# Optimization experiments

Measured on AMD Instinct MI355X. Metric: run time of the kernel, lower is better.

Reference implementation:

```python
import jax, jax.numpy as jnp
import numpy as np
import math

K = 2
CAPACITY = -1
NEED_L_AUX = True


def topk_gating(logits, k=K, capacity=CAPACITY, need_l_aux=NEED_L_AUX):
    # logits: (T, P, E) tokens x prototypes x experts-per-prototype
    gates = jax.nn.softmax(logits.astype(jnp.float32), axis=-1).astype(logits.dtype)
    T, P, E = gates.shape
    cap = int(math.ceil(1.25 * T / E)) if capacity < 0 else capacity

    idx1 = jnp.argmax(gates, axis=-1)                      # (T, P)
    mask1 = jax.nn.one_hot(idx1, E, dtype=jnp.int32)       # (T, P, E)
    loc1 = jnp.cumsum(mask1, axis=0) - 1                   # position in expert queue
    if need_l_aux:
        me = jnp.mean(gates, axis=0)
        ce = jnp.mean(mask1.astype(jnp.float32), axis=0)
        l_aux = jnp.mean(me * ce)
    else:
        l_aux = jnp.zeros((), jnp.float32)
    mask1 = mask1 * (loc1 < cap)                           # drop over-capacity tokens
    loc1_s = jnp.sum(loc1 * mask1, axis=-1)                # (T, P)
    gates1_s = jnp.sum(gates * mask1, axis=-1)
    denom = gates1_s
    gates_s_list = [gates1_s]
    mask_list = [mask1]
    loc_s_list = [loc1_s]
    last_logits = logits
    last_mask = mask1
    prev_masks = mask1
    for _ in range(2, k + 1):
        last_logits = jnp.where(last_mask.astype(bool), -jnp.inf, last_logits)
        idx = jnp.argmax(last_logits, axis=-1)
        mask = jax.nn.one_hot(idx, E, dtype=jnp.int32)
        loc = jnp.cumsum(mask, axis=0) - 1 + jnp.sum(prev_masks, axis=0, keepdims=True)
        mask = mask * (loc < cap)
        last_mask = mask
        prev_masks = prev_masks + mask
        mask_list.append(mask)
        loc_s_list.append(jnp.sum(loc * mask, axis=-1))
        gs = jnp.sum(gates * mask, axis=-1)
        denom = denom + gs
        gates_s_list.append(gs)
    denom = jnp.maximum(denom, jnp.finfo(denom.dtype).eps)

    combine = jnp.zeros((T, P, E, cap), gates.dtype)
    for gs, mask, ls in zip(gates_s_list, mask_list, loc_s_list):
        g = (gs / denom)[..., None] * mask                  # (T, P, E)
        loc_sc = jax.nn.one_hot(ls, cap, dtype=gates.dtype)  # (T, P, cap)
        combine = combine + g[..., None] * loc_sc[:, :, None, :]
    dispatch_mask = combine.astype(bool)
    return l_aux.astype(logits.dtype), combine.astype(logits.dtype), dispatch_mask


def setup_inputs() -> dict:
    key = jax.random.key(0)
    k1, k2 = jax.random.split(key)
    inp = jax.random.normal(k1, (4096, 2048), dtype=jnp.float32)
    W = jax.random.normal(k2, (64, 2048), dtype=jnp.float32) / math.sqrt(2048.0)
    return {"input": inp, "W": W, "bs": 4096, "prototypes": 2}


def reference(input, W, bs, prototypes):
    logits = input @ W.T                                   # (T, num_experts_total)
    logits = logits.reshape(input.shape[0], prototypes, -1)  # (T, P, E)
    return topk_gating(logits, k=K, capacity=CAPACITY, need_l_aux=NEED_L_AUX)
```

## Files before the change

### kernel.cpp

```cpp
#include <hip/hip_runtime.h>
#include <cstdint>

#define T_TOK 4096
#define KDIM 2048
#define NE 64
#define NP 2
#define EE 32
#define CAP 160
#define NKC 8
#define KCHUNK 256
#define BLKR 128
#define COMB_ELEMS 41943040ull
#define OUT_ELEMS 83886081ull
#define SMALLF 65536

__global__ __launch_bounds__(256) void k_gemm(const float* __restrict__ x,
                                              const float* __restrict__ W,
                                              float* __restrict__ part) {
  __shared__ float xs[BLKR][36];
  __shared__ float wt[32][68];
  const int tid = threadIdx.x;
  const int rb = blockIdx.x & 31;
  const int kc = blockIdx.x >> 5;
  const int r0 = rb * BLKR;
  const int er = tid & 15;
  const int rg = tid >> 4;
  float acc[8][4];
#pragma unroll
  for (int i = 0; i < 8; ++i)
#pragma unroll
    for (int c = 0; c < 4; ++c) acc[i][c] = 0.f;

  float4 sx[4], sw[2];
  {
    const int kb = kc * KCHUNK;
#pragma unroll
    for (int q = 0; q < 4; ++q) {
      const int li = tid + q * 256, row = li >> 3, kq = (li & 7) * 4;
      sx[q] = *reinterpret_cast<const float4*>(&x[(size_t)(r0 + row) * KDIM + kb + kq]);
    }
#pragma unroll
    for (int q = 0; q < 2; ++q) {
      const int li = tid + q * 256, e = li >> 3, kq = (li & 7) * 4;
      sw[q] = *reinterpret_cast<const float4*>(&W[(size_t)e * KDIM + kb + kq]);
    }
  }
  for (int s = 0; s < 8; ++s) {
    __syncthreads();
#pragma unroll
    for (int q = 0; q < 4; ++q) {
      const int li = tid + q * 256, row = li >> 3, kq = (li & 7) * 4;
      *reinterpret_cast<float4*>(&xs[row][kq]) = sx[q];
    }
#pragma unroll
    for (int q = 0; q < 2; ++q) {
      const int li = tid + q * 256, e = li >> 3, kq = (li & 7) * 4;
      wt[kq][e] = sw[q].x; wt[kq + 1][e] = sw[q].y;
      wt[kq + 2][e] = sw[q].z; wt[kq + 3][e] = sw[q].w;
    }
    if (s < 7) {
      const int kb = kc * KCHUNK + (s + 1) * 32;
#pragma unroll
      for (int q = 0; q < 4; ++q) {
        const int li = tid + q * 256, row = li >> 3, kq = (li & 7) * 4;
        sx[q] = *reinterpret_cast<const float4*>(&x[(size_t)(r0 + row) * KDIM + kb + kq]);
      }
#pragma unroll
      for (int q = 0; q < 2; ++q) {
        const int li = tid + q * 256, e = li >> 3, kq = (li & 7) * 4;
        sw[q] = *reinterpret_cast<const float4*>(&W[(size_t)e * KDIM + kb + kq]);
      }
    }
    __syncthreads();
#pragma unroll
    for (int k4 = 0; k4 < 8; ++k4) {
      float4 wb[4];
#pragma unroll
      for (int j = 0; j < 4; ++j)
        wb[j] = *reinterpret_cast<const float4*>(&wt[k4 * 4 + j][er * 4]);
#pragma unroll
      for (int i = 0; i < 8; ++i) {
        const float4 xv = *reinterpret_cast<const float4*>(&xs[rg + 16 * i][k4 * 4]);
        acc[i][0] = fmaf(xv.w, wb[3].x, fmaf(xv.z, wb[2].x, fmaf(xv.y, wb[1].x, fmaf(xv.x, wb[0].x, acc[i][0]))));
        acc[i][1] = fmaf(xv.w, wb[3].y, fmaf(xv.z, wb[2].y, fmaf(xv.y, wb[1].y, fmaf(xv.x, wb[0].y, acc[i][1]))));
        acc[i][2] = fmaf(xv.w, wb[3].z, fmaf(xv.z, wb[2].z, fmaf(xv.y, wb[1].z, fmaf(xv.x, wb[0].z, acc[i][2]))));
        acc[i][3] = fmaf(xv.w, wb[3].w, fmaf(xv.z, wb[2].w, fmaf(xv.y, wb[1].w, fmaf(xv.x, wb[0].w, acc[i][3]))));
      }
    }
  }
#pragma unroll
  for (int i = 0; i < 8; ++i) {
    float4 v; v.x = acc[i][0]; v.y = acc[i][1]; v.z = acc[i][2]; v.w = acc[i][3];
    *reinterpret_cast<float4*>(
        &part[((size_t)kc * T_TOK + r0 + rg + 16 * i) * NE + er * 4]) = v;
  }
}

__global__ __launch_bounds__(64) void k_soft(const float* __restrict__ part,
                                             float2* __restrict__ g12,
                                             int* __restrict__ idxs,
                                             float* __restrict__ me_part) {
  __shared__ float lg[64][33];
  const int tid = threadIdx.x;
  const int R = blockIdx.x * 64 + tid;
  const int t = R >> 1;
  const int p = R & 1;
  float v[32];
  const float* pr = part + (size_t)t * NE + p * EE;
#pragma unroll
  for (int e = 0; e < 32; e += 4) {
    float4 s = *reinterpret_cast<const float4*>(pr + e);
    v[e] = s.x; v[e + 1] = s.y; v[e + 2] = s.z; v[e + 3] = s.w;
  }
  for (int kc = 1; kc < NKC; ++kc) {
    const float* prk = pr + (size_t)kc * T_TOK * NE;
#pragma unroll
    for (int e = 0; e < 32; e += 4) {
      float4 s = *reinterpret_cast<const float4*>(prk + e);
      v[e] += s.x; v[e + 1] += s.y; v[e + 2] += s.z; v[e + 3] += s.w;
    }
  }
  float m = v[0];
#pragma unroll
  for (int e = 1; e < 32; ++e) m = fmaxf(m, v[e]);
  float sum = 0.f;
#pragma unroll
  for (int e = 0; e < 32; ++e) { v[e] = expf(v[e] - m); sum += v[e]; }
  const float inv = 1.0f / sum;
#pragma unroll
  for (int e = 0; e < 32; ++e) v[e] *= inv;
  float g1 = -1.f; int i1 = 0;
#pragma unroll
  for (int e = 0; e < 32; ++e) if (v[e] > g1) { g1 = v[e]; i1 = e; }
  float g2 = -1.f; int i2 = 0;
#pragma unroll
  for (int e = 0; e < 32; ++e) if (e != i1 && v[e] > g2) { g2 = v[e]; i2 = e; }
  g12[R] = make_float2(g1, g2);
  idxs[R] = i1 | (i2 << 8);
#pragma unroll
  for (int e = 0; e < 32; ++e) lg[tid][e] = v[e];
  __syncthreads();
  {
    const int pp = tid >> 5, ee = tid & 31;
    float s = 0.f;
    for (int rr = pp; rr < 64; rr += 2) s += lg[rr][ee];
    me_part[blockIdx.x * 64 + tid] = s;
  }
}

__global__ __launch_bounds__(1024) void k_scan(const int* __restrict__ idxs,
                                               const float2* __restrict__ g12,
                                               const float* __restrict__ me_part,
                                               int2* __restrict__ fl,
                                               float2* __restrict__ wvp,
                                               float* __restrict__ out) {
  __shared__ int grp[NP][64][32];
  __shared__ int tot[NP][32];
  __shared__ unsigned short tk1[NP][T_TOK];
  __shared__ unsigned short tk2[NP][T_TOK];
  __shared__ float red[64];
  const int tid = threadIdx.x;
  const int wvi = tid >> 6;
  const int p = wvi >> 3;
  const int wg = wvi & 7;
  const int l = tid & 63;
  const unsigned long long lmask = (1ull << l) - 1ull;
  for (int gi = 0; gi < 8; ++gi) {
    const int g = wg * 8 + gi;
    const int t = g * 64 + l;
    const int e1 = idxs[t * 2 + p] & 255;
    if (l < 32) grp[p][g][l] = 0;
    unsigned long long m = ~0ull;
#pragma unroll
    for (int b = 0; b < 5; ++b) {
      const unsigned long long bm = __ballot((e1 >> b) & 1);
      m &= ((e1 >> b) & 1) ? bm : ~bm;
    }
    const int rank = (int)__popcll(m & lmask);
    if (rank == 0) grp[p][g][e1] = (int)__popcll(m);
    tk1[p][t] = (unsigned short)(rank | (e1 << 6));
  }
  __syncthreads();
  if (tid < 64) {
    const int pp = tid >> 5, ee = tid & 31;
    int s = 0;
    for (int g = 0; g < 64; ++g) { int vv = grp[pp][g][ee]; grp[pp][g][ee] = s; s += vv; }
    tot[pp][ee] = s;
  }
  __syncthreads();
  for (int gi = 0; gi < 8; ++gi) {
    const int g = wg * 8 + gi;
    const int t = g * 64 + l;
    const int vv = tk1[p][t];
    tk1[p][t] = (unsigned short)(grp[p][g][vv >> 6] + (vv & 63));
  }
  if (tid < 64) {
    float s = 0.f;
    for (int b = 0; b < 128; ++b) s += me_part[b * 64 + tid];
    red[tid] = s * (float)tot[tid >> 5][tid & 31];
  }
  __syncthreads();
  if (tid == 0) {
    float s = 0.f;
    for (int i = 0; i < 64; ++i) s += red[i];
    out[0] = s / (64.0f * 4096.0f * 4096.0f);
  }
  for (int gi = 0; gi < 8; ++gi) {
    const int g = wg * 8 + gi;
    const int t = g * 64 + l;
    const int ii = idxs[t * 2 + p];
    const int e2 = (tk1[p][t] < CAP) ? (ii >> 8) : (ii & 255);
    if (l < 32) grp[p][g][l] = 0;
    unsigned long long m = ~0ull;
#pragma unroll
    for (int b = 0; b < 5; ++b) {
      const unsigned long long bm = __ballot((e2 >> b) & 1);
      m &= ((e2 >> b) & 1) ? bm : ~bm;
    }
    const int rank = (int)__popcll(m & lmask);
    if (rank == 0) grp[p][g][e2] = (int)__popcll(m);
    tk2[p][t] = (unsigned short)(rank | (e2 << 6));
  }
  __syncthreads();
  if (tid < 64) {
    const int pp = tid >> 5, ee = tid & 31;
    int s = min(tot[pp][ee], CAP);
    for (int g = 0; g < 64; ++g) { int vv = grp[pp][g][ee]; grp[pp][g][ee] = s; s += vv; }
  }
  __syncthreads();
  for (int gi = 0; gi < 8; ++gi) {
    const int g = wg * 8 + gi;
    const int t = g * 64 + l;
    const int R = t * 2 + p;
    const int ii = idxs[R];
    const int e1 = ii & 255;
    const int loc1v = tk1[p][t];
    const bool kept1 = loc1v < CAP;
    const int v2 = tk2[p][t];
    const int rank2 = v2 & 63, e2 = v2 >> 6;
    const int loc2 = grp[p][g][e2] + rank2;
    const bool kept2 = loc2 < CAP;
    const float2 gg = g12[R];
    const float gs1 = kept1 ? gg.x : 0.f;
    const float g2v = kept1 ? gg.y : gg.x;
    const float gs2 = kept2 ? g2v : 0.f;
    const float den = fmaxf(gs1 + gs2, 1.1920929e-07f);
    fl[R] = make_int2(kept1 ? e1 * CAP + loc1v : -1, kept2 ? e2 * CAP + loc2 : -1);
    wvp[R] = make_float2(gs1 / den, gs2 / den);
  }
}

__global__ __launch_bounds__(256) void k_write(const int2* __restrict__ fl,
                                               const float2* __restrict__ wvp,
                                               float* __restrict__ out,
                                               int nfullB) {
  const int b = blockIdx.x;
  const int tid = threadIdx.x;
  const int region = b >> 12;
  const int bd = b & 4095;
  if (region && bd >= nfullB) return;
  int fpos = -1; float fval = 0.f; size_t faddr = 0;
  if (tid < 4) {
    const int rr = 2 * bd + (tid >> 1);
    const int2 f = fl[rr];
    const float2 w = wvp[rr];
    const int which = tid & 1;
    fpos = which ? f.y : f.x;
    fval = region ? 1.0f : (which ? w.y : w.x);
    faddr = 1ull + (region ? COMB_ELEMS : 0ull) + (size_t)rr * 5120 + (size_t)(fpos < 0 ? 0 : fpos);
  }
  const size_t base = 1 + (region ? COMB_ELEMS : 0ull) + (size_t)bd * 10240;
  float4* p4 = (float4*)(out + base + 3);
  const float4 z4 = make_float4(0.f, 0.f, 0.f, 0.f);
#pragma unroll
  for (int j = 0; j < 10; ++j) {
    const int idx = tid + j * 256;
    if (idx < 2559) p4[idx] = z4;
  }
  if (tid < 3) out[base + tid] = 0.f;
  if (tid == 3) out[base + 10239] = 0.f;
  __syncthreads();
  if (tid < 4 && fpos >= 0) out[faddr] = fval;
}

__global__ __launch_bounds__(1024) void k_write_tail(const int2* __restrict__ fl,
                                                     float* __restrict__ out,
                                                     int nfullB) {
  __shared__ int2 sfl[16];
  const int tid = threadIdx.x;
  const int rstart = nfullB * 2;
  const int nr = 8192 - rstart;
  if (tid < nr) sfl[tid] = fl[rstart + tid];
  __syncthreads();
  const size_t base = 1 + COMB_ELEMS + (size_t)rstart * 5120;
  const int cnt = nr * 5120;
  const int nx4 = (cnt - 4) >> 2;
  float4* p4 = (float4*)(out + base + 3);
  const float4 z4 = make_float4(0.f, 0.f, 0.f, 0.f);
  for (int idx = tid; idx < nx4; idx += 1024) p4[idx] = z4;
  if (tid < 3) out[base + tid] = 0.f;
  if (tid == 3) out[base + cnt - 1] = 0.f;
  __syncthreads();
  if (tid < 2 * nr) {
    const int rr = rstart + (tid >> 1);
    const int2 f = sfl[tid >> 1];
    const int pos = (tid & 1) ? f.y : f.x;
    if (pos >= 0) out[1 + COMB_ELEMS + (size_t)rr * 5120 + pos] = 1.0f;
  }
}

extern "C" void kernel_launch(void* const* d_in, const int* in_sizes, int n_in,
                              void* d_out, int out_size, void* d_ws, size_t ws_size,
                              hipStream_t stream) {
  const float* x = (const float*)d_in[0];
  const float* W = (const float*)d_in[1];
  float* out = (float*)d_out;

  const size_t PARTF = (size_t)NKC * T_TOK * NE;

  float* small;
  float* part;
  int nfullB = 4096;
  if (ws_size >= (SMALLF + PARTF) * sizeof(float)) {
    small = (float*)d_ws;
    part = small + SMALLF;
  } else if (ws_size >= SMALLF * sizeof(float)) {
    small = (float*)d_ws;
    part = out + 4;
  } else {
    const size_t tb = (OUT_ELEMS - SMALLF) & ~(size_t)3;
    small = out + tb;
    part = out + 4;
    nfullB = (int)((tb - 1 - COMB_ELEMS) / 10240);
  }
  float2* g12 = (float2*)small;
  int* idxs = (int*)(small + 16384);
  float* me_part = small + 24576;
  int2* fl = (int2*)(small + 32768);
  float2* wvp = (float2*)(small + 49152);

  hipLaunchKernelGGL(k_gemm, dim3(256), dim3(256), 0, stream, x, W, part);
  hipLaunchKernelGGL(k_soft, dim3(128), dim3(64), 0, stream, part, g12, idxs, me_part);
  hipLaunchKernelGGL(k_scan, dim3(1), dim3(1024), 0, stream, idxs, g12, me_part, fl, wvp, out);
  hipLaunchKernelGGL(k_write, dim3(8192), dim3(256), 0, stream, fl, wvp, out, nfullB);
  if (nfullB < 4096)
    hipLaunchKernelGGL(k_write_tail, dim3(1), dim3(1024), 0, stream, fl, out, nfullB);
}
```

Measured before the change: 123.3 us.

## Overlap output zero-fill with GEMM blocks and scatter nonzeros in a separate fix kernel

Appends 4096 zero-fill blocks to the GEMM launch so the large combine/dispatch zeroing runs alongside the GEMM instead of after the scan. The old write kernel, which zeroed each row and then wrote the nonzeros, becomes a small scatter kernel that writes only the nonzero entries. Regions of the output that are reused as scratch are skipped and zeroed later by an extra fill kernel. The risks are that fill blocks compete with GEMM blocks for bandwidth and that the scratch aliasing paths are now more complex.

```diff
diff --git a/kernel.cpp b/kernel.cpp
--- a/kernel.cpp
+++ b/kernel.cpp
@@ -13,13 +13,33 @@
 #define COMB_ELEMS 41943040ull
 #define OUT_ELEMS 83886081ull
 #define SMALLF 65536
-
-__global__ __launch_bounds__(256) void k_gemm(const float* __restrict__ x,
-                                              const float* __restrict__ W,
-                                              float* __restrict__ part) {
+#define NFB 4096
+#define TOT4 20971520
+
+__global__ __launch_bounds__(256) void k_fused(const float* __restrict__ x,
+                                               const float* __restrict__ W,
+                                               float* __restrict__ part,
+                                               float* __restrict__ out,
+                                               int s1lo, int s1hi, int s2lo, int s2hi,
+                                               int fillLast) {
   __shared__ float xs[BLKR][36];
   __shared__ float wt[32][68];
   const int tid = threadIdx.x;
+  if (blockIdx.x >= 256) {
+    const int fb = blockIdx.x - 256;
+    float4* p4 = reinterpret_cast<float4*>(out);
+    const float4 z4 = make_float4(0.f, 0.f, 0.f, 0.f);
+    const int start = fb * 5120;
+#pragma unroll
+    for (int j = 0; j < 20; ++j) {
+      const int i4 = start + tid + j * 256;
+      if (i4 >= s1lo && i4 < s1hi) continue;
+      if (i4 >= s2lo && i4 < s2hi) continue;
+      p4[i4] = z4;
+    }
+    if (fillLast && fb == NFB - 1 && tid == 255) out[OUT_ELEMS - 1] = 0.f;
+    return;
+  }
   const int rb = blockIdx.x & 31;
   const int kc = blockIdx.x >> 5;
   const int r0 = rb * BLKR;
@@ -94,6 +114,14 @@
     *reinterpret_cast<float4*>(
         &part[((size_t)kc * T_TOK + r0 + rg + 16 * i) * NE + er * 4]) = v;
   }
+}
+
+__global__ __launch_bounds__(256) void k_fill2(float* __restrict__ out) {
+  float4* p4 = reinterpret_cast<float4*>(out + 4);
+  const float4 z4 = make_float4(0.f, 0.f, 0.f, 0.f);
+  const int base = blockIdx.x * 2048 + threadIdx.x;
+#pragma unroll
+  for (int j = 0; j < 8; ++j) p4[base + j * 256] = z4;
 }
 
 __global__ __launch_bounds__(64) void k_soft(const float* __restrict__ part,
@@ -250,37 +278,21 @@
   }
 }
 
-__global__ __launch_bounds__(256) void k_write(const int2* __restrict__ fl,
-                                               const float2* __restrict__ wvp,
-                                               float* __restrict__ out,
-                                               int nfullB) {
-  const int b = blockIdx.x;
-  const int tid = threadIdx.x;
-  const int region = b >> 12;
-  const int bd = b & 4095;
-  if (region && bd >= nfullB) return;
-  int fpos = -1; float fval = 0.f; size_t faddr = 0;
-  if (tid < 4) {
-    const int rr = 2 * bd + (tid >> 1);
-    const int2 f = fl[rr];
-    const float2 w = wvp[rr];
-    const int which = tid & 1;
-    fpos = which ? f.y : f.x;
-    fval = region ? 1.0f : (which ? w.y : w.x);
-    faddr = 1ull + (region ? COMB_ELEMS : 0ull) + (size_t)rr * 5120 + (size_t)(fpos < 0 ? 0 : fpos);
-  }
-  const size_t base = 1 + (region ? COMB_ELEMS : 0ull) + (size_t)bd * 10240;
-  float4* p4 = (float4*)(out + base + 3);
-  const float4 z4 = make_float4(0.f, 0.f, 0.f, 0.f);
-#pragma unroll
-  for (int j = 0; j < 10; ++j) {
-    const int idx = tid + j * 256;
-    if (idx < 2559) p4[idx] = z4;
-  }
-  if (tid < 3) out[base + tid] = 0.f;
-  if (tid == 3) out[base + 10239] = 0.f;
-  __syncthreads();
-  if (tid < 4 && fpos >= 0) out[faddr] = fval;
+__global__ __launch_bounds__(256) void k_fix(const int2* __restrict__ fl,
+                                             const float2* __restrict__ wvp,
+                                             float* __restrict__ out,
+                                             int rlimit) {
+  const int R = blockIdx.x * 256 + threadIdx.x;
+  const int2 f = fl[R];
+  const float2 w = wvp[R];
+  float* oc = out + 1 + (size_t)R * 5120;
+  if (f.x >= 0) oc[f.x] = w.x;
+  if (f.y >= 0) oc[f.y] = w.y;
+  if (R < rlimit) {
+    float* od = out + 1 + COMB_ELEMS + (size_t)R * 5120;
+    if (f.x >= 0) od[f.x] = 1.0f;
+    if (f.y >= 0) od[f.y] = 1.0f;
+  }
 }
 
 __global__ __launch_bounds__(1024) void k_write_tail(const int2* __restrict__ fl,
@@ -320,18 +332,27 @@
 
   float* small;
   float* part;
-  int nfullB = 4096;
+  int s1lo = 0, s1hi = 0, s2lo = 0, s2hi = 0, fillLast = 1;
+  bool needFill2 = false;
+  int nfullB = 4096, rlimit = 8192;
   if (ws_size >= (SMALLF + PARTF) * sizeof(float)) {
     small = (float*)d_ws;
     part = small + SMALLF;
   } else if (ws_size >= SMALLF * sizeof(float)) {
     small = (float*)d_ws;
     part = out + 4;
+    s1lo = 1; s1hi = 1 + (int)(PARTF / 4);
+    needFill2 = true;
   } else {
     const size_t tb = (OUT_ELEMS - SMALLF) & ~(size_t)3;
     small = out + tb;
     part = out + 4;
+    s1lo = 1; s1hi = 1 + (int)(PARTF / 4);
+    s2lo = (int)(tb / 4); s2hi = TOT4;
+    fillLast = 0;
+    needFill2 = true;
     nfullB = (int)((tb - 1 - COMB_ELEMS) / 10240);
+    rlimit = nfullB * 2;
   }
   float2* g12 = (float2*)small;
   int* idxs = (int*)(small + 16384);
@@ -339,10 +360,13 @@
   int2* fl = (int2*)(small + 32768);
   float2* wvp = (float2*)(small + 49152);
 
-  hipLaunchKernelGGL(k_gemm, dim3(256), dim3(256), 0, stream, x, W, part);
+  hipLaunchKernelGGL(k_fused, dim3(256 + NFB), dim3(256), 0, stream,
+                     x, W, part, out, s1lo, s1hi, s2lo, s2hi, fillLast);
   hipLaunchKernelGGL(k_soft, dim3(128), dim3(64), 0, stream, part, g12, idxs, me_part);
+  if (needFill2)
+    hipLaunchKernelGGL(k_fill2, dim3(256), dim3(256), 0, stream, out);
   hipLaunchKernelGGL(k_scan, dim3(1), dim3(1024), 0, stream, idxs, g12, me_part, fl, wvp, out);
-  hipLaunchKernelGGL(k_write, dim3(8192), dim3(256), 0, stream, fl, wvp, out, nfullB);
+  hipLaunchKernelGGL(k_fix, dim3(32), dim3(256), 0, stream, fl, wvp, out, rlimit);
   if (nfullB < 4096)
     hipLaunchKernelGGL(k_write_tail, dim3(1), dim3(1024), 0, stream, fl, out, nfullB);
 }
```

Measured after the change: 104.0 us. 15.7% less time.
